# Optimization experiments

Measured on AMD Instinct MI355X. Metric: run time of the kernel, lower is better.

The kernel has to match this reference:

```python
import jax, jax.numpy as jnp
import numpy as np

K = 5  # spline kernel size per dim (dim=3 -> 125 kernels)
NS = [20000, 5000, 1280, 320, 80, 32, 16]
ES = [320000, 80000, 20480, 5120, 1280, 512]
NF = [2, 16, 32, 64, 128, 128, 128]

_BITS = jnp.array([[(b >> d) & 1 for d in range(3)] for b in range(8)], dtype=jnp.int32)  # [8,3]
_STRIDES = jnp.array([1, K, K * K], dtype=jnp.int32)


def spline_conv(x, edge_index, pseudo, W, root, bias):
    """SplineConv, dim=3, kernel_size=5, degree-1 open B-splines, mean aggregation.
    x: [N,Cin], edge_index: [2,E], pseudo: [E,3] in [0,1], W: [125,Cin,Cout]."""
    N, Cin = x.shape
    src, dst = edge_index[0], edge_index[1]
    p = pseudo * (K - 1)                                  # [E,3]
    k0 = jnp.clip(jnp.floor(p), 0.0, K - 2)
    frac = p - k0                                         # [E,3]
    k0 = k0.astype(jnp.int32)
    # degree-1 basis: 2^3 = 8 active kernel corners per edge
    w = jnp.where(_BITS[None] == 1, frac[:, None, :], 1.0 - frac[:, None, :])  # [E,8,3]
    wprod = jnp.prod(w, axis=-1)                          # [E,8]
    kidx = jnp.sum((k0[:, None, :] + _BITS[None]) * _STRIDES, axis=-1)         # [E,8]
    xj = x[src]                                           # gather [E,Cin]
    # scatter weighted source features into (dst node, kernel) buckets
    seg = (dst[:, None] * (K ** 3) + kidx).reshape(-1)    # [E*8]
    contrib = (wprod[..., None] * xj[:, None, :]).reshape(-1, Cin)
    A = jax.ops.segment_sum(contrib, seg, num_segments=N * K ** 3).reshape(N, K ** 3, Cin)
    out = jnp.einsum('nki,kio->no', A, W)                 # [N,Cout]
    deg = jax.ops.segment_sum(jnp.ones(src.shape[0], x.dtype), dst, num_segments=N)
    out = out / jnp.maximum(deg, 1.0)[:, None]            # mean aggregation
    return out + x @ root + bias                          # root weight + bias


def _forward(x, eis, eas, Ps, Ws, Rs, bs):
    for l in range(6):
        h = jax.nn.elu(spline_conv(x, eis[l], eas[l], Ws[l], Rs[l], bs[l]))
        x = Ps[l].T @ h                                   # pool to coarser mesh
    return jnp.max(x, axis=0)[None, :]                    # AdaptiveMaxPool1d(1) over nodes -> [1,128]


def setup_inputs() -> dict:
    key = jax.random.key(0)
    ks = iter(jax.random.split(key, 64))
    inp = {"x": jax.random.normal(next(ks), (NS[0], NF[0]), jnp.float32)}
    for l in range(6):
        inp[f"ei{l}"] = jax.random.randint(next(ks), (2, ES[l]), 0, NS[l], dtype=jnp.int32)
        inp[f"ea{l}"] = jax.random.uniform(next(ks), (ES[l], 3), jnp.float32)
    pnames = ["P01", "P12", "P23", "P34", "P45", "P56"]
    for l, pn in enumerate(pnames):
        inp[pn] = jax.random.normal(next(ks), (NS[l], NS[l + 1]), jnp.float32) * (NS[l] ** -0.5)
    for l in range(6):
        cin, cout = NF[l], NF[l + 1]
        inp[f"W{l+1}"] = jax.random.normal(next(ks), (K ** 3, cin, cout), jnp.float32) * 0.05
        inp[f"R{l+1}"] = jax.random.normal(next(ks), (cin, cout), jnp.float32) * (cin ** -0.5)
        inp[f"b{l+1}"] = jnp.zeros((cout,), jnp.float32)
    return inp


def reference(x, ei0, ea0, ei1, ea1, ei2, ea2, ei3, ea3, ei4, ea4, ei5, ea5,
              P01, P12, P23, P34, P45, P56,
              W1, R1, b1, W2, R2, b2, W3, R3, b3,
              W4, R4, b4, W5, R5, b5, W6, R6, b6):
    eis = [ei0, ei1, ei2, ei3, ei4, ei5]
    eas = [ea0, ea1, ea2, ea3, ea4, ea5]
    Ps = [P01, P12, P23, P34, P45, P56]
    Ws = [W1, W2, W3, W4, W5, W6]
    Rs = [R1, R2, R3, R4, R5, R6]
    bs = [b1, b2, b3, b4, b5, b6]
    return _forward(x, eis, eas, Ps, Ws, Rs, bs)
```

## Files before the change

### kernel.cpp

```cpp
#include <hip/hip_runtime.h>
#include <math.h>

#define NKER 125
#define CAP 64

struct Ptr6i { const int* p[6]; };
struct Ptr6f { const float* p[6]; };

__global__ __launch_bounds__(256) void fill_all_kernel(
    Ptr6i eis, Ptr6f eas, int* __restrict__ cnt, float4* __restrict__ recS) {
  static const int EB[7] = {0, 1250, 1563, 1643, 1663, 1668, 1670};
  static const int Es[6] = {320000, 80000, 20480, 5120, 1280, 512};
  static const int hOff[6] = {0, 20000, 25000, 26280, 26600, 26680};
  int b = blockIdx.x;
  int l = 0;
  while (b >= EB[l + 1]) l++;
  int e = (b - EB[l]) * 256 + threadIdx.x;
  if (e >= Es[l]) return;
  const int* ei = eis.p[l];
  const float* ea = eas.p[l];
  int src = ei[e];
  int dst = ei[Es[l] + e];
  int kpk = 0;
  float f[3];
#pragma unroll
  for (int d = 0; d < 3; d++) {
    float p = ea[e * 3 + d] * 4.0f;
    float kf = fminf(fmaxf(floorf(p), 0.0f), 3.0f);
    f[d] = p - kf;
    kpk |= ((int)kf) << (4 * d);
  }
  int node = hOff[l] + dst;
  int r = atomicAdd(&cnt[node], 1);
  if (r < CAP)
    recS[(size_t)node * CAP + r] =
        make_float4(__uint_as_float((unsigned)src | ((unsigned)kpk << 15)), f[0], f[1], f[2]);
}

template <int CINSH, int G, int KDIM, int KSG, int NT>
__global__ __launch_bounds__(NT) void build4_kernel(
    const int* __restrict__ cntL, const float4* __restrict__ rc,
    const float* __restrict__ x, float* __restrict__ A) {
  __shared__ float rows[G * KDIM];
  const int Cin = 1 << CINSH;
  int tid = threadIdx.x;
  int n0 = blockIdx.x * G;
  for (int t = tid; t < G * KDIM / 4; t += NT)
    ((float4*)rows)[t] = make_float4(0.0f, 0.0f, 0.0f, 0.0f);
  __syncthreads();
  int nl = tid >> CINSH;
  int ci = tid & (Cin - 1);
  int n = n0 + nl;
  int m = min(cntL[n], CAP);
  const float4* re = rc + (size_t)n * CAP;
  float* row = rows + nl * KDIM + ci;
  for (int i = 0; i < m; i++) {
    float4 rec = re[i];
    unsigned v = __float_as_uint(rec.x);
    int src = v & 0x7fff;
    int kpk = v >> 15;
    float f0 = rec.y, f1 = rec.z, f2 = rec.w;
    float xv = x[((size_t)src << CINSH) + ci];
    float g0 = 1.0f - f0, g1 = 1.0f - f1, g2 = 1.0f - f2;
    int kb = (kpk & 15) + 5 * ((kpk >> 4) & 15) + 25 * ((kpk >> 8) & 15);
    float* rb = row + (kb << CINSH);
    rb[0]              += (g0 * g1 * g2) * xv;
    rb[1 << CINSH]     += (f0 * g1 * g2) * xv;
    rb[5 << CINSH]     += (g0 * f1 * g2) * xv;
    rb[6 << CINSH]     += (f0 * f1 * g2) * xv;
    rb[25 << CINSH]    += (g0 * g1 * f2) * xv;
    rb[26 << CINSH]    += (f0 * g1 * f2) * xv;
    rb[30 << CINSH]    += (g0 * f1 * f2) * xv;
    rb[31 << CINSH]    += (f0 * f1 * f2) * xv;
  }
  __syncthreads();
  const int RQ = KSG / 4;
  for (int t = tid; t < G * RQ; t += NT) {
    int r = t / RQ, c4 = t % RQ;
    int c = c4 * 4;
    float4 v = make_float4(0.0f, 0.0f, 0.0f, 0.0f);
    if (c < KDIM) v = *(const float4*)&rows[r * KDIM + c];
    ((float4*)&A[(size_t)(n0 + r) * KSG])[c4] = v;
  }
}

__global__ __launch_bounds__(128) void build4_l0_kernel(
    const int* __restrict__ cntL, const float4* __restrict__ rc,
    const float* __restrict__ x, float* __restrict__ A, int N) {
  __shared__ float rows[64 * 254];
  int tid = threadIdx.x;
  int n0 = blockIdx.x * 64;
  for (int t = tid; t < 64 * 254 / 4; t += 128)
    ((float4*)rows)[t] = make_float4(0.0f, 0.0f, 0.0f, 0.0f);
  __syncthreads();
  int nl = tid >> 1;
  int ci = tid & 1;
  int n = n0 + nl;
  if (n < N) {
    int m = min(cntL[n], CAP);
    const float4* re = rc + (size_t)n * CAP;
    float* row = rows + nl * 254 + ci;
    for (int i = 0; i < m; i++) {
      float4 rec = re[i];
      unsigned v = __float_as_uint(rec.x);
      int src = v & 0x7fff;
      int kpk = v >> 15;
      float f0 = rec.y, f1 = rec.z, f2 = rec.w;
      float xv = x[(size_t)src * 2 + ci];
      float g0 = 1.0f - f0, g1 = 1.0f - f1, g2 = 1.0f - f2;
      int kb = (kpk & 15) + 5 * ((kpk >> 4) & 15) + 25 * ((kpk >> 8) & 15);
      float* rb = row + kb * 2;
      rb[0]  = fmaf(g0 * g1 * g2, xv, rb[0]);
      rb[2]  = fmaf(f0 * g1 * g2, xv, rb[2]);
      rb[10] = fmaf(g0 * f1 * g2, xv, rb[10]);
      rb[12] = fmaf(f0 * f1 * g2, xv, rb[12]);
      rb[50] = fmaf(g0 * g1 * f2, xv, rb[50]);
      rb[52] = fmaf(f0 * g1 * f2, xv, rb[52]);
      rb[60] = fmaf(g0 * f1 * f2, xv, rb[60]);
      rb[62] = fmaf(f0 * f1 * f2, xv, rb[62]);
    }
  }
  __syncthreads();
  for (int it = 0; it < 32; it++) {
    int sub = tid >> 6;
    int c4 = tid & 63;
    int nn = n0 + it * 2 + sub;
    if (nn >= N) continue;
    float4 v = make_float4(0.0f, 0.0f, 0.0f, 0.0f);
    if (c4 < 63) v = *(const float4*)&rows[(it * 2 + sub) * 254 + c4 * 4];
    ((float4*)&A[(size_t)nn * 256])[c4] = v;
  }
}

template <int BM, int COUT, int NT>
__global__ __launch_bounds__(NT) void gemm3_kernel(
    const float* __restrict__ A, const float* __restrict__ W,
    float* __restrict__ gpart, int M, int Kdim, int KS, int ktiles) {
  const int BK = 32;
  __shared__ float At[BK][BM + 4];
  __shared__ float Wl[BK][COUT];
  const int TC = COUT / 4;
  int tid = threadIdx.x;
  int tc = tid % TC;
  int tr = tid / TC;
  int m0 = blockIdx.x * BM;
  int kbeg = blockIdx.y * ktiles * BK;
  int kend = min(KS, kbeg + ktiles * BK);
  float ar[4][4];
#pragma unroll
  for (int i = 0; i < 4; i++)
#pragma unroll
    for (int j = 0; j < 4; j++) ar[i][j] = 0.0f;

  for (int k0 = kbeg; k0 < kend; k0 += BK) {
    for (int t = tid; t < BM * (BK / 4); t += NT) {
      int c4 = t % (BK / 4), r = t / (BK / 4);
      int m = m0 + r;
      float4 v = make_float4(0.0f, 0.0f, 0.0f, 0.0f);
      if (m < M) v = *(const float4*)&A[(size_t)m * KS + k0 + c4 * 4];
      At[c4 * 4 + 0][r] = v.x; At[c4 * 4 + 1][r] = v.y;
      At[c4 * 4 + 2][r] = v.z; At[c4 * 4 + 3][r] = v.w;
    }
    int kleft = Kdim - k0;
    if (kleft >= BK) {
      for (int t = tid; t < BK * COUT / 4; t += NT)
        ((float4*)&Wl[0][0])[t] = ((const float4*)&W[(size_t)k0 * COUT])[t];
    } else {
      for (int t = tid; t < BK * COUT; t += NT) {
        int kk = t / COUT, o = t % COUT;
        Wl[kk][o] = (kk < kleft) ? W[(size_t)(k0 + kk) * COUT + o] : 0.0f;
      }
    }
    __syncthreads();
#pragma unroll
    for (int kk = 0; kk < BK; kk++) {
      float4 a = *(const float4*)&At[kk][tr * 4];
      float4 w = *(const float4*)&Wl[kk][tc * 4];
      float av[4] = {a.x, a.y, a.z, a.w};
      float wv[4] = {w.x, w.y, w.z, w.w};
#pragma unroll
      for (int i = 0; i < 4; i++)
#pragma unroll
        for (int j = 0; j < 4; j++)
          ar[i][j] = fmaf(av[i], wv[j], ar[i][j]);
    }
    __syncthreads();
  }
  float* gp = gpart + ((size_t)blockIdx.y * M) * COUT + tc * 4;
#pragma unroll
  for (int i = 0; i < 4; i++) {
    int m = m0 + tr * 4 + i;
    if (m < M)
      *(float4*)(gp + (size_t)m * COUT) =
          make_float4(ar[i][0], ar[i][1], ar[i][2], ar[i][3]);
  }
}

__global__ __launch_bounds__(256) void epilogue_kernel(
    const float* __restrict__ gpart, const int* __restrict__ degI,
    const float* __restrict__ x, const float* __restrict__ R,
    const float* __restrict__ b, float* __restrict__ h,
    int N, int Cin, int coutShift, int kchunks) {
  int tid = blockIdx.x * 256 + threadIdx.x;
  int Cout = 1 << coutShift;
  if (tid >= (N << coutShift)) return;
  int n = tid >> coutShift;
  int o = tid & (Cout - 1);
  size_t stride = (size_t)N << coutShift;
  float s = 0.0f;
  for (int c = 0; c < kchunks; c++) s += gpart[(size_t)c * stride + tid];
  s /= (float)max(degI[n], 1);
  float r = b[o];
  const float* xr = &x[n * Cin];
  for (int i = 0; i < Cin; i++) r = fmaf(xr[i], R[i * Cout + o], r);
  float v = s + r;
  h[tid] = v > 0.0f ? v : expm1f(v);
}

#define FMA4(c, pj, h) \
  c.x = fmaf(pj, h.x, c.x); c.y = fmaf(pj, h.y, c.y); \
  c.z = fmaf(pj, h.z, c.z); c.w = fmaf(pj, h.w, c.w);

template <int COUT, int OPT>
__global__ __launch_bounds__(256) void pool5c_kernel(
    const float* __restrict__ P, const float* __restrict__ h,
    float* __restrict__ partial, int Nsrc, int Nnext, int chunk, int items) {
  extern __shared__ float hs[];
  int c = blockIdx.y;
  int n0 = c * chunk;
  int n1 = min(Nsrc, n0 + chunk);
  int len = n1 - n0;
  for (int t = threadIdx.x; t < len * (COUT / 4); t += 256)
    ((float4*)hs)[t] = ((const float4*)&h[(size_t)n0 * COUT])[t];
  __syncthreads();
  int item = blockIdx.x * 256 + threadIdx.x;
  if (item >= items) return;
  int nj4 = Nnext >> 2;
  int j0 = (item % nj4) << 2;
  int o0 = (item / nj4) * OPT;
  const float4 z = make_float4(0.0f, 0.0f, 0.0f, 0.0f);
  float4 c00 = z, c01 = z, c02 = z, c03 = z;
  float4 c10 = z, c11 = z, c12 = z, c13 = z;
  float4 c20 = z, c21 = z, c22 = z, c23 = z;
  float4 c30 = z, c31 = z, c32 = z, c33 = z;
  const float* Pb = P + j0;

#define USTEP(pv, nn)                                                    \
  {                                                                      \
    const float4* hr = (const float4*)&hs[(nn) * COUT + o0];             \
    float4 h0 = hr[0], h1 = hr[1];                                       \
    FMA4(c00, pv.x, h0) FMA4(c01, pv.x, h1)                              \
    FMA4(c10, pv.y, h0) FMA4(c11, pv.y, h1)                              \
    FMA4(c20, pv.z, h0) FMA4(c21, pv.z, h1)                              \
    FMA4(c30, pv.w, h0) FMA4(c31, pv.w, h1)                              \
    if constexpr (OPT == 16) {                                           \
      float4 h2 = hr[2], h3 = hr[3];                                     \
      FMA4(c02, pv.x, h2) FMA4(c03, pv.x, h3)                            \
      FMA4(c12, pv.y, h2) FMA4(c13, pv.y, h3)                            \
      FMA4(c22, pv.z, h2) FMA4(c23, pv.z, h3)                            \
      FMA4(c32, pv.w, h2) FMA4(c33, pv.w, h3)                            \
    }                                                                    \
  }

  int n = 0;
  for (; n + 8 <= len; n += 8) {
    float4 pv0 = *(const float4*)&Pb[(size_t)(n0 + n + 0) * Nnext];
    float4 pv1 = *(const float4*)&Pb[(size_t)(n0 + n + 1) * Nnext];
    float4 pv2 = *(const float4*)&Pb[(size_t)(n0 + n + 2) * Nnext];
    float4 pv3 = *(const float4*)&Pb[(size_t)(n0 + n + 3) * Nnext];
    float4 pv4 = *(const float4*)&Pb[(size_t)(n0 + n + 4) * Nnext];
    float4 pv5 = *(const float4*)&Pb[(size_t)(n0 + n + 5) * Nnext];
    float4 pv6 = *(const float4*)&Pb[(size_t)(n0 + n + 6) * Nnext];
    float4 pv7 = *(const float4*)&Pb[(size_t)(n0 + n + 7) * Nnext];
    USTEP(pv0, n + 0)
    USTEP(pv1, n + 1)
    USTEP(pv2, n + 2)
    USTEP(pv3, n + 3)
    USTEP(pv4, n + 4)
    USTEP(pv5, n + 5)
    USTEP(pv6, n + 6)
    USTEP(pv7, n + 7)
  }
  for (; n < len; n++) {
    float4 pv = *(const float4*)&Pb[(size_t)(n0 + n) * Nnext];
    USTEP(pv, n)
  }
#undef USTEP

  float* pp = partial + ((size_t)c * Nnext + j0) * COUT + o0;
  *(float4*)(pp + 0 * COUT + 0) = c00;
  *(float4*)(pp + 0 * COUT + 4) = c01;
  *(float4*)(pp + 1 * COUT + 0) = c10;
  *(float4*)(pp + 1 * COUT + 4) = c11;
  *(float4*)(pp + 2 * COUT + 0) = c20;
  *(float4*)(pp + 2 * COUT + 4) = c21;
  *(float4*)(pp + 3 * COUT + 0) = c30;
  *(float4*)(pp + 3 * COUT + 4) = c31;
  if constexpr (OPT == 16) {
    *(float4*)(pp + 0 * COUT + 8)  = c02;
    *(float4*)(pp + 0 * COUT + 12) = c03;
    *(float4*)(pp + 1 * COUT + 8)  = c12;
    *(float4*)(pp + 1 * COUT + 12) = c13;
    *(float4*)(pp + 2 * COUT + 8)  = c22;
    *(float4*)(pp + 2 * COUT + 12) = c23;
    *(float4*)(pp + 3 * COUT + 8)  = c32;
    *(float4*)(pp + 3 * COUT + 12) = c33;
  }
}

__global__ __launch_bounds__(256) void preduce_kernel(
    const float* __restrict__ partial, float* __restrict__ xnext,
    int NnCout, int chunks) {
  int i = blockIdx.x * 256 + threadIdx.x;
  if (i >= NnCout) return;
  float s = 0.0f;
  for (int c = 0; c < chunks; c++) s += partial[(size_t)c * NnCout + i];
  xnext[i] = s;
}

__global__ __launch_bounds__(128) void max_kernel(const float* __restrict__ x6,
                                                  float* __restrict__ out) {
  int o = threadIdx.x;
  float m = -3.0e38f;
  for (int n = 0; n < 16; n++) m = fmaxf(m, x6[n * 128 + o]);
  out[o] = m;
}

extern "C" void kernel_launch(void* const* d_in, const int* in_sizes, int n_in,
                              void* d_out, int out_size, void* d_ws, size_t ws_size,
                              hipStream_t stream) {
  static const int NSh[7] = {20000, 5000, 1280, 320, 80, 32, 16};
  static const int NFh[7] = {2, 16, 32, 64, 128, 128, 128};
  static const int cinSh[6]  = {1, 4, 5, 6, 7, 7};
  static const int coutSh[6] = {4, 5, 6, 7, 7, 7};
  static const int KSt[6] = {256, 2016, 4000, 8000, 16000, 16000};
  static const int kchunksTab[6] = {4, 8, 16, 32, 64, 128};
  static const int ktilesTab[6]  = {2, 8, 8, 8, 8, 4};
  static const int poolChunksTab[6] = {120, 80, 16, 8, 4, 2};
  static const int histOff[6] = {0, 20000, 25000, 26280, 26600, 26680};

  const float* x0 = (const float*)d_in[0];
  Ptr6i eis;
  Ptr6f eas;
  for (int l = 0; l < 6; l++) {
    eis.p[l] = (const int*)d_in[1 + 2 * l];
    eas.p[l] = (const float*)d_in[2 + 2 * l];
  }
  const float* Pm[6];
  for (int l = 0; l < 6; l++) Pm[l] = (const float*)d_in[13 + l];
  const float* Wt[6];
  const float* Rt[6];
  const float* bt[6];
  for (int l = 0; l < 6; l++) {
    Wt[l] = (const float*)d_in[19 + 3 * l];
    Rt[l] = (const float*)d_in[20 + 3 * l];
    bt[l] = (const float*)d_in[21 + 3 * l];
  }

  float* ws = (float*)d_ws;
  float* A     = ws;
  float* gpart = ws + 10150000;
  float* hbuf  = ws + 11500000;
  float* ppart = ws + 12000000;
  float* xA    = ws + 32100000;
  float* xB    = ws + 32200000;
  int* cnt     = (int*)(ws + 32300000);
  float4* recS = (float4*)(ws + 33000000);

  hipMemsetAsync(cnt, 0, 26712 * sizeof(int), stream);
  fill_all_kernel<<<1670, 256, 0, stream>>>(eis, eas, cnt, recS);

  const float* cur = x0;
  for (int l = 0; l < 6; l++) {
    int N = NSh[l], Nn = NSh[l + 1], Cin = NFh[l], Cout = NFh[l + 1];
    int Kdim = NKER * Cin, KS = KSt[l];
    float* xnext = (l & 1) ? xB : xA;
    const int* cntL = cnt + histOff[l];
    const float4* rc = recS + (size_t)histOff[l] * CAP;

    switch (l) {
      case 0: build4_l0_kernel<<<313, 128, 0, stream>>>(cntL, rc, cur, A, N); break;
      case 1: build4_kernel<4, 8, 2000, 2016, 128><<<625, 128, 0, stream>>>(cntL, rc, cur, A); break;
      case 2: build4_kernel<5, 4, 4000, 4000, 128><<<320, 128, 0, stream>>>(cntL, rc, cur, A); break;
      case 3: build4_kernel<6, 2, 8000, 8000, 128><<<160, 128, 0, stream>>>(cntL, rc, cur, A); break;
      case 4: build4_kernel<7, 1, 16000, 16000, 128><<<80, 128, 0, stream>>>(cntL, rc, cur, A); break;
      default: build4_kernel<7, 1, 16000, 16000, 128><<<32, 128, 0, stream>>>(cntL, rc, cur, A); break;
    }

    int kchunks = kchunksTab[l], ktiles = ktilesTab[l];
    switch (l) {
      case 0: {
        dim3 g((N + 127) / 128, kchunks);
        gemm3_kernel<128, 16, 128><<<g, 128, 0, stream>>>(A, Wt[l], gpart, N, Kdim, KS, ktiles);
        break;
      }
      case 1: {
        dim3 g((N + 127) / 128, kchunks);
        gemm3_kernel<128, 32, 256><<<g, 256, 0, stream>>>(A, Wt[l], gpart, N, Kdim, KS, ktiles);
        break;
      }
      case 2: {
        dim3 g((N + 63) / 64, kchunks);
        gemm3_kernel<64, 64, 256><<<g, 256, 0, stream>>>(A, Wt[l], gpart, N, Kdim, KS, ktiles);
        break;
      }
      default: {
        dim3 g((N + 31) / 32, kchunks);
        gemm3_kernel<32, 128, 256><<<g, 256, 0, stream>>>(A, Wt[l], gpart, N, Kdim, KS, ktiles);
        break;
      }
    }

    int ethreads = N << coutSh[l];
    epilogue_kernel<<<(ethreads + 255) / 256, 256, 0, stream>>>(
        gpart, cntL, cur, Rt[l], bt[l], hbuf, N, Cin, coutSh[l], kchunks);

    int pc = poolChunksTab[l];
    int chunk = (N + pc - 1) / pc;
    size_t ldsB = (size_t)chunk * Cout * sizeof(float);
    int items, gx;
    switch (Cout) {
      case 16:
        items = (Nn >> 2) * 1;
        gx = (items + 255) / 256;
        pool5c_kernel<16, 16><<<dim3(gx, pc), 256, ldsB, stream>>>(Pm[l], hbuf, ppart, N, Nn, chunk, items);
        break;
      case 32:
        items = (Nn >> 2) * 2;
        gx = (items + 255) / 256;
        pool5c_kernel<32, 16><<<dim3(gx, pc), 256, ldsB, stream>>>(Pm[l], hbuf, ppart, N, Nn, chunk, items);
        break;
      case 64:
        items = (Nn >> 2) * 8;
        gx = (items + 255) / 256;
        pool5c_kernel<64, 8><<<dim3(gx, pc), 256, ldsB, stream>>>(Pm[l], hbuf, ppart, N, Nn, chunk, items);
        break;
      default:
        items = (Nn >> 2) * 16;
        gx = (items + 255) / 256;
        pool5c_kernel<128, 8><<<dim3(gx, pc), 256, ldsB, stream>>>(Pm[l], hbuf, ppart, N, Nn, chunk, items);
        break;
    }
    int NnCout = Nn << coutSh[l];
    preduce_kernel<<<(NnCout + 255) / 256, 256, 0, stream>>>(ppart, xnext, NnCout, pc);

    cur = xnext;
  }

  max_kernel<<<1, 128, 0, stream>>>(cur, (float*)d_out);
}
```

Measured before the change: 690.7 us.

## Fuse layer-0 spline conv into one direct kernel; retune split-K for deep layers

Layer 0 (Cin=2, Cout=16) previously built a dense [N,256] bucket matrix, ran a split-K GEMM, then a separate epilogue. Now a single kernel does this per node: it keeps W in shared memory, applies each edge's 8 spline corners straight to the 16 output accumulators, and finishes with mean, root, bias and ELU. This removes three launches and the A/gpart round trips through global memory, at the cost of more FMAs per edge and one thread per node, which can be unbalanced when degrees vary. The split-K chunk and tile counts for layers 4 and 5 are also changed.

```diff
diff --git a/kernel.cpp b/kernel.cpp
--- a/kernel.cpp
+++ b/kernel.cpp
@@ -35,6 +35,60 @@
   if (r < CAP)
     recS[(size_t)node * CAP + r] =
         make_float4(__uint_as_float((unsigned)src | ((unsigned)kpk << 15)), f[0], f[1], f[2]);
+}
+
+__global__ __launch_bounds__(128) void conv0_kernel(
+    const int* __restrict__ cnt, const float4* __restrict__ rc,
+    const float* __restrict__ x, const float* __restrict__ W,
+    const float* __restrict__ R, const float* __restrict__ bias,
+    float* __restrict__ h, int N) {
+  __shared__ float Wl[125 * 33 + 48];
+  int tid = threadIdx.x;
+  for (int t = tid; t < 4000; t += 128) {
+    int k = t >> 5, rem = t & 31;
+    Wl[k * 33 + rem] = W[t];
+  }
+  if (tid < 32) Wl[4125 + tid] = R[tid];
+  if (tid < 16) Wl[4157 + tid] = bias[tid];
+  __syncthreads();
+  int n = blockIdx.x * 128 + tid;
+  if (n >= N) return;
+  int deg = cnt[n];
+  int m = min(deg, CAP);
+  const float4* re = rc + (size_t)n * CAP;
+  float acc[16];
+#pragma unroll
+  for (int o = 0; o < 16; o++) acc[o] = 0.0f;
+  for (int i = 0; i < m; i++) {
+    float4 rec = re[i];
+    unsigned v = __float_as_uint(rec.x);
+    int src = v & 0x7fff;
+    int kpk = v >> 15;
+    float f0 = rec.y, f1 = rec.z, f2 = rec.w;
+    float x0 = x[(size_t)src * 2], x1 = x[(size_t)src * 2 + 1];
+    float g0 = 1.0f - f0, g1 = 1.0f - f1, g2 = 1.0f - f2;
+    int kb = (kpk & 15) + 5 * ((kpk >> 4) & 15) + 25 * ((kpk >> 8) & 15);
+#pragma unroll
+    for (int c = 0; c < 8; c++) {
+      int b0 = c & 1, b1 = (c >> 1) & 1, b2 = c >> 2;
+      float wp = (b0 ? f0 : g0) * (b1 ? f1 : g1) * (b2 ? f2 : g2);
+      int kidx = kb + b0 + 5 * b1 + 25 * b2;
+      const float* Wb = &Wl[kidx * 33];
+      float wx0 = wp * x0, wx1 = wp * x1;
+#pragma unroll
+      for (int o = 0; o < 16; o++)
+        acc[o] = fmaf(wx0, Wb[o], fmaf(wx1, Wb[16 + o], acc[o]));
+    }
+  }
+  float invd = 1.0f / (float)max(deg, 1);
+  float xa = x[(size_t)n * 2], xb = x[(size_t)n * 2 + 1];
+  float* hp = h + (size_t)n * 16;
+#pragma unroll
+  for (int o = 0; o < 16; o++) {
+    float r = Wl[4157 + o] + xa * Wl[4125 + o] + xb * Wl[4125 + 16 + o];
+    float vv = fmaf(acc[o], invd, r);
+    hp[o] = vv > 0.0f ? vv : expm1f(vv);
+  }
 }
 
 template <int CINSH, int G, int KDIM, int KSG, int NT>
@@ -84,54 +138,6 @@
   }
 }
 
-__global__ __launch_bounds__(128) void build4_l0_kernel(
-    const int* __restrict__ cntL, const float4* __restrict__ rc,
-    const float* __restrict__ x, float* __restrict__ A, int N) {
-  __shared__ float rows[64 * 254];
-  int tid = threadIdx.x;
-  int n0 = blockIdx.x * 64;
-  for (int t = tid; t < 64 * 254 / 4; t += 128)
-    ((float4*)rows)[t] = make_float4(0.0f, 0.0f, 0.0f, 0.0f);
-  __syncthreads();
-  int nl = tid >> 1;
-  int ci = tid & 1;
-  int n = n0 + nl;
-  if (n < N) {
-    int m = min(cntL[n], CAP);
-    const float4* re = rc + (size_t)n * CAP;
-    float* row = rows + nl * 254 + ci;
-    for (int i = 0; i < m; i++) {
-      float4 rec = re[i];
-      unsigned v = __float_as_uint(rec.x);
-      int src = v & 0x7fff;
-      int kpk = v >> 15;
-      float f0 = rec.y, f1 = rec.z, f2 = rec.w;
-      float xv = x[(size_t)src * 2 + ci];
-      float g0 = 1.0f - f0, g1 = 1.0f - f1, g2 = 1.0f - f2;
-      int kb = (kpk & 15) + 5 * ((kpk >> 4) & 15) + 25 * ((kpk >> 8) & 15);
-      float* rb = row + kb * 2;
-      rb[0]  = fmaf(g0 * g1 * g2, xv, rb[0]);
-      rb[2]  = fmaf(f0 * g1 * g2, xv, rb[2]);
-      rb[10] = fmaf(g0 * f1 * g2, xv, rb[10]);
-      rb[12] = fmaf(f0 * f1 * g2, xv, rb[12]);
-      rb[50] = fmaf(g0 * g1 * f2, xv, rb[50]);
-      rb[52] = fmaf(f0 * g1 * f2, xv, rb[52]);
-      rb[60] = fmaf(g0 * f1 * f2, xv, rb[60]);
-      rb[62] = fmaf(f0 * f1 * f2, xv, rb[62]);
-    }
-  }
-  __syncthreads();
-  for (int it = 0; it < 32; it++) {
-    int sub = tid >> 6;
-    int c4 = tid & 63;
-    int nn = n0 + it * 2 + sub;
-    if (nn >= N) continue;
-    float4 v = make_float4(0.0f, 0.0f, 0.0f, 0.0f);
-    if (c4 < 63) v = *(const float4*)&rows[(it * 2 + sub) * 254 + c4 * 4];
-    ((float4*)&A[(size_t)nn * 256])[c4] = v;
-  }
-}
-
 template <int BM, int COUT, int NT>
 __global__ __launch_bounds__(NT) void gemm3_kernel(
     const float* __restrict__ A, const float* __restrict__ W,
@@ -334,8 +340,8 @@
   static const int cinSh[6]  = {1, 4, 5, 6, 7, 7};
   static const int coutSh[6] = {4, 5, 6, 7, 7, 7};
   static const int KSt[6] = {256, 2016, 4000, 8000, 16000, 16000};
-  static const int kchunksTab[6] = {4, 8, 16, 32, 64, 128};
-  static const int ktilesTab[6]  = {2, 8, 8, 8, 8, 4};
+  static const int kchunksTab[6] = {4, 8, 16, 32, 32, 64};
+  static const int ktilesTab[6]  = {2, 8, 8, 8, 16, 8};
   static const int poolChunksTab[6] = {120, 80, 16, 8, 4, 2};
   static const int histOff[6] = {0, 20000, 25000, 26280, 26600, 26680};
 
@@ -378,42 +384,39 @@
     const int* cntL = cnt + histOff[l];
     const float4* rc = recS + (size_t)histOff[l] * CAP;
 
-    switch (l) {
-      case 0: build4_l0_kernel<<<313, 128, 0, stream>>>(cntL, rc, cur, A, N); break;
-      case 1: build4_kernel<4, 8, 2000, 2016, 128><<<625, 128, 0, stream>>>(cntL, rc, cur, A); break;
-      case 2: build4_kernel<5, 4, 4000, 4000, 128><<<320, 128, 0, stream>>>(cntL, rc, cur, A); break;
-      case 3: build4_kernel<6, 2, 8000, 8000, 128><<<160, 128, 0, stream>>>(cntL, rc, cur, A); break;
-      case 4: build4_kernel<7, 1, 16000, 16000, 128><<<80, 128, 0, stream>>>(cntL, rc, cur, A); break;
-      default: build4_kernel<7, 1, 16000, 16000, 128><<<32, 128, 0, stream>>>(cntL, rc, cur, A); break;
-    }
-
-    int kchunks = kchunksTab[l], ktiles = ktilesTab[l];
-    switch (l) {
-      case 0: {
-        dim3 g((N + 127) / 128, kchunks);
-        gemm3_kernel<128, 16, 128><<<g, 128, 0, stream>>>(A, Wt[l], gpart, N, Kdim, KS, ktiles);
-        break;
+    if (l == 0) {
+      conv0_kernel<<<(N + 127) / 128, 128, 0, stream>>>(
+          cntL, rc, cur, Wt[0], Rt[0], bt[0], hbuf, N);
+    } else {
+      switch (l) {
+        case 1: build4_kernel<4, 8, 2000, 2016, 128><<<625, 128, 0, stream>>>(cntL, rc, cur, A); break;
+        case 2: build4_kernel<5, 4, 4000, 4000, 128><<<320, 128, 0, stream>>>(cntL, rc, cur, A); break;
+        case 3: build4_kernel<6, 2, 8000, 8000, 128><<<160, 128, 0, stream>>>(cntL, rc, cur, A); break;
+        case 4: build4_kernel<7, 1, 16000, 16000, 128><<<80, 128, 0, stream>>>(cntL, rc, cur, A); break;
+        default: build4_kernel<7, 1, 16000, 16000, 128><<<32, 128, 0, stream>>>(cntL, rc, cur, A); break;
       }
-      case 1: {
-        dim3 g((N + 127) / 128, kchunks);
-        gemm3_kernel<128, 32, 256><<<g, 256, 0, stream>>>(A, Wt[l], gpart, N, Kdim, KS, ktiles);
-        break;
+      int kchunks = kchunksTab[l], ktiles = ktilesTab[l];
+      switch (l) {
+        case 1: {
+          dim3 g((N + 127) / 128, kchunks);
+          gemm3_kernel<128, 32, 256><<<g, 256, 0, stream>>>(A, Wt[l], gpart, N, Kdim, KS, ktiles);
+          break;
+        }
+        case 2: {
+          dim3 g((N + 63) / 64, kchunks);
+          gemm3_kernel<64, 64, 256><<<g, 256, 0, stream>>>(A, Wt[l], gpart, N, Kdim, KS, ktiles);
+          break;
+        }
+        default: {
+          dim3 g((N + 31) / 32, kchunks);
+          gemm3_kernel<32, 128, 256><<<g, 256, 0, stream>>>(A, Wt[l], gpart, N, Kdim, KS, ktiles);
+          break;
+        }
       }
-      case 2: {
-        dim3 g((N + 63) / 64, kchunks);
-        gemm3_kernel<64, 64, 256><<<g, 256, 0, stream>>>(A, Wt[l], gpart, N, Kdim, KS, ktiles);
-        break;
-      }
-      default: {
-        dim3 g((N + 31) / 32, kchunks);
-        gemm3_kernel<32, 128, 256><<<g, 256, 0, stream>>>(A, Wt[l], gpart, N, Kdim, KS, ktiles);
-        break;
-      }
-    }
-
-    int ethreads = N << coutSh[l];
-    epilogue_kernel<<<(ethreads + 255) / 256, 256, 0, stream>>>(
-        gpart, cntL, cur, Rt[l], bt[l], hbuf, N, Cin, coutSh[l], kchunks);
+      int ethreads = N << coutSh[l];
+      epilogue_kernel<<<(ethreads + 255) / 256, 256, 0, stream>>>(
+          gpart, cntL, cur, Rt[l], bt[l], hbuf, N, Cin, coutSh[l], kchunks);
+    }
 
     int pc = poolChunksTab[l];
     int chunk = (N + pc - 1) / pc;
```

Result: slower. 720.5 us (+4.3%).
